# Optimization experiments

Measured on AMD Instinct MI355X. Metric: run time of the kernel, lower is better.

## Reference

```python
import jax, jax.numpy as jnp
import numpy as np

NUM_BRANCHES = 4
REP_DIM = 1024
FEAT_DIM = 128
N_DATA = 100000
NCE_K = 4096
NCE_T = 0.07
BATCH = 128
EPS = 1e-07


def setup_inputs() -> dict:
    key = jax.random.key(0)
    ks = jax.random.split(key, 8)
    d = {}
    for i in range(NUM_BRANCHES):
        d[f"emb{i}"] = jax.random.normal(ks[i], (BATCH, REP_DIM), dtype=jnp.float32)
    d["W"] = jax.random.normal(ks[4], (NUM_BRANCHES, FEAT_DIM, REP_DIM), dtype=jnp.float32) * 0.03
    d["b"] = jnp.zeros((NUM_BRANCHES, FEAT_DIM), dtype=jnp.float32)
    stdv = 1.0 / np.sqrt(FEAT_DIM / 3.0)
    d["memory"] = jax.random.uniform(ks[5], (NUM_BRANCHES, N_DATA, FEAT_DIM), dtype=jnp.float32, minval=-stdv, maxval=stdv)
    idx = jax.random.randint(ks[6], (BATCH,), 0, N_DATA)
    neg = jax.random.randint(ks[7], (BATCH, NCE_K), 0, N_DATA)
    d["idx"] = idx
    d["contrast_idx"] = jnp.concatenate([idx[:, None], neg], axis=1)  # col 0 = positive
    return d


def reference(emb0, emb1, emb2, emb3, W, b, memory, idx, contrast_idx):
    # per-branch Embed: flatten -> Linear -> L2 normalize
    embs = jnp.stack([emb0, emb1, emb2, emb3], axis=0)            # [R,B,rep]
    h = jnp.einsum('rbi,rdi->rbd', embs, W) + b[:, None, :]        # [R,B,D]
    e = h / jnp.sqrt(jnp.sum(h * h, axis=-1, keepdims=True))       # Normalize(power=2)

    # ContrastMemory: gather K+1 bank rows per sample per branch (detached)
    w = jax.lax.stop_gradient(memory[:, contrast_idx, :])          # [R,B,K+1,D]
    # scores[i,j,b,k] = <bank_j row, emb_i>  for every ordered pair
    scores = jnp.einsum('jbkd,ibd->ijbk', w, e)                    # [R,R,B,K+1]
    out = jnp.exp(scores / NCE_T)
    Z = jax.lax.stop_gradient(jnp.mean(out, axis=(2, 3)) * N_DATA)  # per-pair Z estimate
    out = out / Z[:, :, None, None]

    # ContrastLoss (Eq 11)
    m = float(NCE_K)
    Pn = 1.0 / float(N_DATA)
    pos = out[:, :, :, 0]                                          # [R,R,B]
    neg = out[:, :, :, 1:]                                         # [R,R,B,K]
    log_D1 = jnp.log(pos / (pos + m * Pn + EPS))
    log_D0 = jnp.log((m * Pn) / (neg + m * Pn + EPS))
    per_pair = -(jnp.sum(log_D1, axis=2) + jnp.sum(log_D0, axis=(2, 3))) / BATCH
    mask = 1.0 - jnp.eye(NUM_BRANCHES, dtype=per_pair.dtype)       # only i != j pairs
    return jnp.sum(per_pair * mask)
```

## Files before the change

kernel.cpp:

```cpp
#include <hip/hip_runtime.h>
#include <math.h>

#define NBR    4
#define REP    1024
#define FD     128
#define NDATA  100000
#define KP1    4097
#define BN     128
#define MPN    0.04096f
#define EPS_C  1e-7f
#define TINV   (1.0f / 0.07f)
#define NSLOT  64
#define TREFS  (BN * KP1)
#define NWAVE  8192

typedef unsigned int   uint4e   __attribute__((ext_vector_type(4)));
typedef unsigned short ushort4e __attribute__((ext_vector_type(4)));
typedef _Float16       half2e   __attribute__((ext_vector_type(2)));
typedef float          floatx4  __attribute__((ext_vector_type(4)));

static __device__ __forceinline__ unsigned short f2h(float f) {
    union { _Float16 h; unsigned short u; } c; c.h = (_Float16)f; return c.u;
}
static __device__ __forceinline__ float h_lo(unsigned int u) {
    union { unsigned int u; _Float16 h[2]; } c; c.u = u; return (float)c.h[0];
}
static __device__ __forceinline__ float h_hi(unsigned int u) {
    union { unsigned int u; _Float16 h[2]; } c; c.u = u; return (float)c.h[1];
}
static __device__ __forceinline__ half2e u2h2(unsigned int u) {
    union { unsigned int u; half2e h; } c; c.u = u; return c.h;
}
static __device__ __forceinline__ unsigned short f2bf(float f) {
    union { float f; unsigned int u; } c; c.f = f;
    unsigned int u = c.u;
    u += 0x7fffu + ((u >> 16) & 1u);
    return (unsigned short)(u >> 16);
}
static __device__ __forceinline__ float bf2f(unsigned short h) {
    union { unsigned int u; float f; } c; c.u = ((unsigned int)h) << 16;
    return c.f;
}

__global__ void k_feat(const float* __restrict__ e0, const float* __restrict__ e1,
                       const float* __restrict__ e2, const float* __restrict__ e3,
                       const float* __restrict__ W, const float* __restrict__ bias,
                       float* __restrict__ e_out, ushort* __restrict__ eh16) {
    const int r = blockIdx.x;
    const int b = blockIdx.y;
    const float* emb = (r == 0 ? e0 : r == 1 ? e1 : r == 2 ? e2 : e3) + (size_t)b * REP;

    __shared__ float s_emb[REP];
    for (int i = threadIdx.x; i < REP; i += blockDim.x) s_emb[i] = emb[i];
    __syncthreads();

    const int d = threadIdx.x;
    const float4* wrow = (const float4*)(W + ((size_t)r * FD + d) * REP);
    float acc = 0.f;
#pragma unroll 8
    for (int c = 0; c < REP / 4; ++c) {
        float4 v = wrow[c];
        acc += v.x * s_emb[4*c+0] + v.y * s_emb[4*c+1]
             + v.z * s_emb[4*c+2] + v.w * s_emb[4*c+3];
    }
    float h = acc + bias[r * FD + d];

    __shared__ float red[FD];
    red[d] = h * h;
    __syncthreads();
    for (int off = FD / 2; off > 0; off >>= 1) {
        if (d < off) red[d] += red[d + off];
        __syncthreads();
    }
    float nrm = sqrtf(red[0]);
    float val = h / nrm;
    e_out[((size_t)r * BN + b) * FD + d] = val;
    if (eh16) eh16[((size_t)r * BN + b) * FD + d] = f2h(val);
}

__global__ void k_hist(const int* __restrict__ cidx, int* __restrict__ counts) {
    const int k = blockIdx.x * 256 + threadIdx.x;
    if (k >= KP1) return;
    const int b = blockIdx.y;
    atomicAdd(&counts[cidx[(size_t)b * KP1 + k]], 1);
}

__global__ void k_assign(const int* __restrict__ counts, int* __restrict__ start,
                         int* __restrict__ cursor) {
    __shared__ int s[256];
    __shared__ int sbase;
    const int tid = threadIdx.x;
    const int n = blockIdx.x * 256 + tid;
    int c = (n < NDATA) ? counts[n] : 0;
    s[tid] = c;
    __syncthreads();
#pragma unroll
    for (int off = 1; off < 256; off <<= 1) {
        int v = (tid >= off) ? s[tid - off] : 0;
        __syncthreads();
        s[tid] += v;
        __syncthreads();
    }
    if (tid == 255) sbase = atomicAdd(cursor, s[255]);
    __syncthreads();
    if (n < NDATA) start[n] = sbase + s[tid] - c;
}

__global__ void k_scatter(const int* __restrict__ cidx, const int* __restrict__ start,
                          int* __restrict__ fill, unsigned long long* __restrict__ inv64) {
    const int k = blockIdx.x * 256 + threadIdx.x;
    if (k >= KP1) return;
    const int b = blockIdx.y;
    const int n = cidx[(size_t)b * KP1 + k];
    const int pos = atomicAdd(&fill[n], 1);
    inv64[(size_t)start[n] + pos] =
        ((unsigned long long)(unsigned int)n << 20) |
        ((unsigned long long)(unsigned int)b << 13) |
        (unsigned long long)(unsigned int)k;
}

__global__ __launch_bounds__(256)
void k_pass1i(const float* __restrict__ mem, const ushort* __restrict__ eh16,
              const unsigned long long* __restrict__ inv64,
              float* __restrict__ Zsl, ushort* __restrict__ expS) {
    const int lane = threadIdx.x & 63;
    const int w    = threadIdx.x >> 6;
    const int g    = (blockIdx.x << 2) + w;
    const int l4   = lane & 15;
    const int jj   = lane >> 4;
    const int d0   = l4 * 8;
    const bool b3  = (l4 & 8) != 0;
    const bool b2  = (l4 & 4) != 0;

    const int base = g * 64 + (g < 128 ? g : 128);
    const int end  = base + 64 + (g < 128 ? 1 : 0);

    const float* mrow_base = mem + (size_t)jj * NDATA * FD + d0;
    const ushort* eb_base  = eh16 + d0;

    float z = 0.f;
    int n_prev = -1;
    half2e mh[4];
    mh[0] = half2e{(_Float16)0.f, (_Float16)0.f};
    mh[1] = mh[0]; mh[2] = mh[0]; mh[3] = mh[0];

    unsigned long long vnext = inv64[base];
    for (int c = base; c < end; ++c) {
        const unsigned long long v = vnext;
        if (c + 1 < end) vnext = inv64[c + 1];
        const int n = (int)(v >> 20);
        const unsigned int bk = (unsigned int)v & 0xFFFFFu;
        const int b = (int)(bk >> 13);
        const int k = (int)(bk & 8191u);

        const ushort* eb = eb_base + (size_t)b * FD;
        uint4 ev0 = *(const uint4*)(eb);
        uint4 ev1 = *(const uint4*)(eb + (size_t)1 * BN * FD);
        uint4 ev2 = *(const uint4*)(eb + (size_t)2 * BN * FD);
        uint4 ev3 = *(const uint4*)(eb + (size_t)3 * BN * FD);

        if (n != n_prev) {
            const floatx4* mp = (const floatx4*)(mrow_base + (size_t)n * FD);
            floatx4 v0 = __builtin_nontemporal_load(mp);
            floatx4 v1 = __builtin_nontemporal_load(mp + 1);
            mh[0] = half2e{(_Float16)v0.x, (_Float16)v0.y};
            mh[1] = half2e{(_Float16)v0.z, (_Float16)v0.w};
            mh[2] = half2e{(_Float16)v1.x, (_Float16)v1.y};
            mh[3] = half2e{(_Float16)v1.z, (_Float16)v1.w};
            n_prev = n;
        }

        float a0 = 0.f, a1 = 0.f, a2 = 0.f, a3 = 0.f;
#pragma unroll
        for (int q = 0; q < 4; ++q) {
            half2e hw = mh[q];
            a0 = __builtin_amdgcn_fdot2(hw, u2h2((&ev0.x)[q]), a0, false);
            a1 = __builtin_amdgcn_fdot2(hw, u2h2((&ev1.x)[q]), a1, false);
            a2 = __builtin_amdgcn_fdot2(hw, u2h2((&ev2.x)[q]), a2, false);
            a3 = __builtin_amdgcn_fdot2(hw, u2h2((&ev3.x)[q]), a3, false);
        }
        float t0 = __shfl_xor(b3 ? a0 : a2, 8, 64);
        float t1 = __shfl_xor(b3 ? a1 : a3, 8, 64);
        float c0 = (b3 ? a2 : a0) + t0;
        float c1 = (b3 ? a3 : a1) + t1;
        float t2 = __shfl_xor(b2 ? c0 : c1, 4, 64);
        float d  = (b2 ? c1 : c0) + t2;
        d += __shfl_xor(d, 2, 64);
        d += __shfl_xor(d, 1, 64);
        float x = __expf(d * TINV);
        z += x;
        if ((lane & 3) == 0)
            expS[((size_t)b * KP1 + k) * 16 + (lane >> 2)] = f2h(x);
    }

    __shared__ float s_z[4][16];
    const int i = ((l4 >> 3) << 1) | ((l4 >> 2) & 1);
    if ((lane & 3) == 0) s_z[w][i * 4 + jj] = z;
    __syncthreads();
    if (threadIdx.x < 16) {
        float vv = s_z[0][threadIdx.x] + s_z[1][threadIdx.x]
                 + s_z[2][threadIdx.x] + s_z[3][threadIdx.x];
        const int slot = blockIdx.x & (NSLOT - 1);
        atomicAdd(&Zsl[slot * 16 + threadIdx.x], vv);
    }
}

__global__ void k_zred(const float* __restrict__ Zsl, float* __restrict__ Zsum) {
    if (threadIdx.x < 16) {
        float s = 0.f;
        for (int sl = 0; sl < NSLOT; ++sl) s += Zsl[sl * 16 + threadIdx.x];
        Zsum[threadIdx.x] = s;
    }
}

static __device__ __forceinline__ void acc_words(const uint4& p0, const uint4& p1,
                                                 const float* __restrict__ s_zinv,
                                                 float* __restrict__ acc, bool pos) {
    unsigned int wds[8] = {p0.x, p0.y, p0.z, p0.w, p1.x, p1.y, p1.z, p1.w};
#pragma unroll
    for (int w = 0; w < 8; ++w) {
        float v0 = h_lo(wds[w]) * s_zinv[2*w];
        float v1 = h_hi(wds[w]) * s_zinv[2*w+1];
        if (pos) {
            acc[2*w]   += -__logf(1.f + (MPN + EPS_C) / v0);
            acc[2*w+1] += -__logf(1.f + (MPN + EPS_C) / v1);
        } else {
            acc[2*w]   += -__logf(1.f + (v0 + EPS_C) * (1.f / MPN));
            acc[2*w+1] += -__logf(1.f + (v1 + EPS_C) * (1.f / MPN));
        }
    }
}

__global__ __launch_bounds__(256)
void k_pass2f(const uint4* __restrict__ expS, const float* __restrict__ Zsum,
              float* __restrict__ Asl) {
    const int b = blockIdx.y;

    __shared__ float s_zinv[16];
    if (threadIdx.x < 16) {
        int jj = threadIdx.x >> 2, ii = threadIdx.x & 3;
        float Z = Zsum[ii * 4 + jj] *
                  (float)((double)NDATA / ((double)BN * (double)KP1));
        s_zinv[threadIdx.x] = 1.0f / Z;
    }
    __syncthreads();

    const uint4* es = expS + (size_t)b * (KP1 * 2);
    const int base = threadIdx.x + blockIdx.x * 256;

    float acc[16];
#pragma unroll
    for (int t = 0; t < 16; ++t) acc[t] = 0.f;

#pragma unroll
    for (int it = 0; it < 2; ++it) {
        const int k = base + it * 2048;
        uint4 p0 = es[(size_t)k * 2];
        uint4 p1 = es[(size_t)k * 2 + 1];
        acc_words(p0, p1, s_zinv, acc, k == 0);
    }
    if (base == 0) {
        uint4 p0 = es[(size_t)4096 * 2];
        uint4 p1 = es[(size_t)4096 * 2 + 1];
        acc_words(p0, p1, s_zinv, acc, false);
    }

#pragma unroll
    for (int t = 0; t < 16; ++t) {
#pragma unroll
        for (int off = 32; off > 0; off >>= 1)
            acc[t] += __shfl_down(acc[t], off, 64);
    }
    __shared__ float s_a[4][16];
    const int w = threadIdx.x >> 6;
    if ((threadIdx.x & 63) == 0) {
#pragma unroll
        for (int t = 0; t < 16; ++t) s_a[w][t] = acc[t];
    }
    __syncthreads();
    if (threadIdx.x < 16) {
        float v = s_a[0][threadIdx.x] + s_a[1][threadIdx.x]
                + s_a[2][threadIdx.x] + s_a[3][threadIdx.x];
        const int slot = (blockIdx.y * gridDim.x + blockIdx.x) & (NSLOT - 1);
        atomicAdd(&Asl[slot * 16 + threadIdx.x], v);
    }
}

__global__ void k_final_slots(const float* __restrict__ Asl, float* __restrict__ out) {
    const int tid = threadIdx.x;
    const int comp = tid & 15;
    const int grp  = tid >> 4;
    float a = 0.f;
    for (int sl = grp; sl < NSLOT; sl += 16) a += Asl[sl * 16 + comp];
    const float m = ((comp >> 2) != (comp & 3)) ? 1.f : 0.f;
    __shared__ float s[256];
    s[tid] = a * m;
    __syncthreads();
    for (int off = 128; off > 0; off >>= 1) {
        if (tid < off) s[tid] += s[tid + off];
        __syncthreads();
    }
    if (tid == 0) out[0] = -s[0] / (float)BN;
}

static __device__ __forceinline__ void dot4(const float4* __restrict__ row,
                                            const float* __restrict__ se,
                                            float& a0, float& a1, float& a2, float& a3) {
    a0 = a1 = a2 = a3 = 0.f;
#pragma unroll 8
    for (int c = 0; c < FD / 4; ++c) {
        float4 v = row[c];
        const int o = 4 * c;
        a0 += v.x * se[0*FD+o+0] + v.y * se[0*FD+o+1] + v.z * se[0*FD+o+2] + v.w * se[0*FD+o+3];
        a1 += v.x * se[1*FD+o+0] + v.y * se[1*FD+o+1] + v.z * se[1*FD+o+2] + v.w * se[1*FD+o+3];
        a2 += v.x * se[2*FD+o+0] + v.y * se[2*FD+o+1] + v.z * se[2*FD+o+2] + v.w * se[2*FD+o+3];
        a3 += v.x * se[3*FD+o+0] + v.y * se[3*FD+o+1] + v.z * se[3*FD+o+2] + v.w * se[3*FD+o+3];
    }
}

static __device__ __forceinline__ void block_reduce4(float z0, float z1, float z2,
                                                     float z3, float* dst, int j) {
    __shared__ float sred[256];
    float zs[NBR] = {z0, z1, z2, z3};
    for (int i = 0; i < NBR; ++i) {
        sred[threadIdx.x] = zs[i];
        __syncthreads();
        for (int off = 128; off > 0; off >>= 1) {
            if ((int)threadIdx.x < off) sred[threadIdx.x] += sred[threadIdx.x + off];
            __syncthreads();
        }
        if (threadIdx.x == 0) atomicAdd(&dst[i * NBR + j], sred[0]);
        __syncthreads();
    }
}

static __device__ __forceinline__ float term_of(float ex, float zinv, int k) {
    const float c = MPN + EPS_C;
    float v = ex * zinv;
    if (k == 0) return -__logf(1.0f + c / v);
    return -__logf(1.0f + (v + EPS_C) * (1.0f / MPN));
}

template <bool STORE>
__global__ void k_pass1_f32(const float* __restrict__ e, const float* __restrict__ memory,
                            const int* __restrict__ cidx,
                            float* __restrict__ Zsum, ushort4* __restrict__ expS) {
    const int j = blockIdx.z;
    const int b = blockIdx.y;

    __shared__ float s_e[NBR * FD];
    for (int t = threadIdx.x; t < NBR * FD; t += blockDim.x) {
        int i = t >> 7, d = t & (FD - 1);
        s_e[t] = e[((size_t)i * BN + b) * FD + d];
    }
    __syncthreads();

    const int* ci = cidx + (size_t)b * KP1;
    const float4* mem4 = (const float4*)(memory + (size_t)j * NDATA * FD);
    float z0 = 0.f, z1 = 0.f, z2 = 0.f, z3 = 0.f;

    for (int k = threadIdx.x + blockIdx.x * blockDim.x; k < KP1;
         k += blockDim.x * gridDim.x) {
        const int n = ci[k];
        const float4* row = mem4 + (size_t)n * (FD / 4);
        float a0, a1, a2, a3;
        dot4(row, s_e, a0, a1, a2, a3);
        float x0 = __expf(a0 * TINV);
        float x1 = __expf(a1 * TINV);
        float x2 = __expf(a2 * TINV);
        float x3 = __expf(a3 * TINV);
        z0 += x0; z1 += x1; z2 += x2; z3 += x3;
        if (STORE) {
            ushort4 st;
            st.x = f2bf(x0); st.y = f2bf(x1); st.z = f2bf(x2); st.w = f2bf(x3);
            expS[((size_t)j * BN + b) * KP1 + k] = st;
        }
    }
    block_reduce4(z0, z1, z2, z3, Zsum, j);
}

__global__ void k_pass2_stored(const ushort4* __restrict__ expS,
                               const float* __restrict__ Zsum,
                               float* __restrict__ accum) {
    const int j = blockIdx.z;
    const int b = blockIdx.y;

    __shared__ float s_zinv[NBR];
    if (threadIdx.x < NBR) {
        float Z = Zsum[threadIdx.x * NBR + j] *
                  (float)((double)NDATA / ((double)BN * (double)KP1));
        s_zinv[threadIdx.x] = 1.0f / Z;
    }
    __syncthreads();

    const ushort4* es = expS + ((size_t)j * BN + b) * KP1;
    float a0 = 0.f, a1 = 0.f, a2 = 0.f, a3 = 0.f;

    for (int k = threadIdx.x + blockIdx.x * blockDim.x; k < KP1;
         k += blockDim.x * gridDim.x) {
        ushort4 v = es[k];
        a0 += term_of(bf2f(v.x), s_zinv[0], k);
        a1 += term_of(bf2f(v.y), s_zinv[1], k);
        a2 += term_of(bf2f(v.z), s_zinv[2], k);
        a3 += term_of(bf2f(v.w), s_zinv[3], k);
    }
    block_reduce4(a0, a1, a2, a3, accum, j);
}

__global__ void k_pass2_regather(const float* __restrict__ e, const float* __restrict__ memory,
                                 const int* __restrict__ cidx,
                                 const float* __restrict__ Zsum, float* __restrict__ accum) {
    const int j = blockIdx.z;
    const int b = blockIdx.y;

    __shared__ float s_e[NBR * FD];
    __shared__ float s_zinv[NBR];
    for (int t = threadIdx.x; t < NBR * FD; t += blockDim.x) {
        int i = t >> 7, d = t & (FD - 1);
        s_e[t] = e[((size_t)i * BN + b) * FD + d];
    }
    if (threadIdx.x < NBR) {
        float Z = Zsum[threadIdx.x * NBR + j] *
                  (float)((double)NDATA / ((double)BN * (double)KP1));
        s_zinv[threadIdx.x] = 1.0f / Z;
    }
    __syncthreads();

    const int* ci = cidx + (size_t)b * KP1;
    const float4* mem4 = (const float4*)(memory + (size_t)j * NDATA * FD);
    float a0s = 0.f, a1s = 0.f, a2s = 0.f, a3s = 0.f;

    for (int k = threadIdx.x + blockIdx.x * blockDim.x; k < KP1;
         k += blockDim.x * gridDim.x) {
        const int n = ci[k];
        const float4* row = mem4 + (size_t)n * (FD / 4);
        float a0, a1, a2, a3;
        dot4(row, s_e, a0, a1, a2, a3);
        a0s += term_of(__expf(a0 * TINV), s_zinv[0], k);
        a1s += term_of(__expf(a1 * TINV), s_zinv[1], k);
        a2s += term_of(__expf(a2 * TINV), s_zinv[2], k);
        a3s += term_of(__expf(a3 * TINV), s_zinv[3], k);
    }
    block_reduce4(a0s, a1s, a2s, a3s, accum, j);
}

__global__ void k_init(float* __restrict__ p, int n) {
    int i = blockIdx.x * blockDim.x + threadIdx.x;
    if (i < n) p[i] = 0.f;
}

__global__ void k_final_legacy(const float* __restrict__ accum, float* __restrict__ out) {
    if (threadIdx.x == 0) {
        float s = 0.f;
        for (int i = 0; i < NBR; ++i)
            for (int j = 0; j < NBR; ++j)
                if (i != j) s += -accum[i * NBR + j] / (float)BN;
        out[0] = s;
    }
}

extern "C" void kernel_launch(void* const* d_in, const int* in_sizes, int n_in,
                              void* d_out, int out_size, void* d_ws, size_t ws_size,
                              hipStream_t stream) {
    const float* e0   = (const float*)d_in[0];
    const float* e1   = (const float*)d_in[1];
    const float* e2   = (const float*)d_in[2];
    const float* e3   = (const float*)d_in[3];
    const float* W    = (const float*)d_in[4];
    const float* bias = (const float*)d_in[5];
    const float* mem  = (const float*)d_in[6];
    const int*   cidx = (const int*)d_in[8];
    float* out = (float*)d_out;

    float* ws    = (float*)d_ws;
    float* e     = ws;
    float* Zsum  = ws + 65536;
    float* accum = ws + 65552;
    float* Zsl   = ws + 65568;
    float* Asl   = ws + 66592;
    const size_t base_b   = (size_t)67616 * 4;
    const size_t eh16_b   = (size_t)NBR * BN * FD * 2;
    const size_t cnt_b    = (size_t)NDATA * 4;
    const size_t cur_b    = 16;
    const size_t inv_b    = (size_t)TREFS * 8;
    const size_t expS_b   = (size_t)BN * KP1 * 16 * 2;

    const size_t off_eh16   = base_b;
    const size_t off_counts = off_eh16 + eh16_b;
    const size_t off_fill   = off_counts + cnt_b;
    const size_t off_cursor = off_fill + cnt_b;
    const size_t off_start  = off_cursor + cur_b;
    const size_t off_inv    = off_start + cnt_b;
    const size_t off_expS   = off_inv + inv_b;

    const size_t need_full = off_expS + expS_b;
    const size_t need_mid  = base_b + expS_b;

    if (ws_size >= need_full) {
        ushort* eh16 = (ushort*)((char*)d_ws + off_eh16);
        int* counts  = (int*)((char*)d_ws + off_counts);
        int* fill    = (int*)((char*)d_ws + off_fill);
        int* cursor  = (int*)((char*)d_ws + off_cursor);
        int* start   = (int*)((char*)d_ws + off_start);
        unsigned long long* inv64 = (unsigned long long*)((char*)d_ws + off_inv);
        ushort* expS = (ushort*)((char*)d_ws + off_expS);

        k_init<<<9, 256, 0, stream>>>(Zsum, 2080);
        k_init<<<782, 256, 0, stream>>>((float*)counts, 200004);
        k_feat<<<dim3(NBR, BN), 128, 0, stream>>>(e0, e1, e2, e3, W, bias, e, eh16);
        k_hist<<<dim3(17, BN), 256, 0, stream>>>(cidx, counts);
        k_assign<<<391, 256, 0, stream>>>(counts, start, cursor);
        k_scatter<<<dim3(17, BN), 256, 0, stream>>>(cidx, start, fill, inv64);
        k_pass1i<<<2048, 256, 0, stream>>>(mem, eh16, inv64, Zsl, expS);
        k_zred<<<1, 64, 0, stream>>>(Zsl, Zsum);
        k_pass2f<<<dim3(8, BN), 256, 0, stream>>>((const uint4*)expS, Zsum, Asl);
        k_final_slots<<<1, 256, 0, stream>>>(Asl, out);
    } else if (ws_size >= need_mid) {
        k_init<<<9, 256, 0, stream>>>(Zsum, 2080);
        k_feat<<<dim3(NBR, BN), 128, 0, stream>>>(e0, e1, e2, e3, W, bias, e, nullptr);
        ushort4* expS = (ushort4*)((char*)d_ws + base_b);
        k_pass1_f32<true><<<dim3(4, BN, NBR), 256, 0, stream>>>(e, mem, cidx, Zsum, expS);
        k_pass2_stored<<<dim3(4, BN, NBR), 256, 0, stream>>>(expS, Zsum, accum);
        k_final_legacy<<<1, 64, 0, stream>>>(accum, out);
    } else {
        k_init<<<9, 256, 0, stream>>>(Zsum, 2080);
        k_feat<<<dim3(NBR, BN), 128, 0, stream>>>(e0, e1, e2, e3, W, bias, e, nullptr);
        k_pass1_f32<false><<<dim3(4, BN, NBR), 256, 0, stream>>>(e, mem, cidx, Zsum, nullptr);
        k_pass2_regather<<<dim3(4, BN, NBR), 256, 0, stream>>>(e, mem, cidx, Zsum, accum);
        k_final_legacy<<<1, 64, 0, stream>>>(accum, out);
    }
}
```

Measured before the change: 484.2 us.

## Fuse setup kernels, store exp scores in sorted order, and software-pipeline pass-1 gathers

The launch sequence goes from ten kernels to six. Init is merged, the feature projection runs in the same launch as the histogram, and the Z reduction and final sum are folded into a single grid-stride pass-2 that adds into the output atomically. Pass-1 now writes exp scores in sorted order, so its stores are contiguous, and it stores embeddings interleaved by branch so that each lane does four contiguous 16-byte loads. It also prefetches two entries ahead, keeping memory rows and embedding vectors in flight. Positives are handled by recording their sorted positions and applying a correction term, which adds some bookkeeping and an order-dependent float atomic sum.

```diff
diff --git a/kernel.cpp b/kernel.cpp
--- a/kernel.cpp
+++ b/kernel.cpp
@@ -12,12 +12,9 @@
 #define TINV   (1.0f / 0.07f)
 #define NSLOT  64
 #define TREFS  (BN * KP1)
-#define NWAVE  8192
-
-typedef unsigned int   uint4e   __attribute__((ext_vector_type(4)));
-typedef unsigned short ushort4e __attribute__((ext_vector_type(4)));
-typedef _Float16       half2e   __attribute__((ext_vector_type(2)));
-typedef float          floatx4  __attribute__((ext_vector_type(4)));
+
+typedef _Float16 half2e  __attribute__((ext_vector_type(2)));
+typedef float    floatx4 __attribute__((ext_vector_type(4)));
 
 static __device__ __forceinline__ unsigned short f2h(float f) {
     union { _Float16 h; unsigned short u; } c; c.h = (_Float16)f; return c.u;
@@ -42,10 +39,337 @@
     return c.f;
 }
 
+__global__ void k_init2(int* __restrict__ cnts, float* __restrict__ Zsl,
+                        float* __restrict__ out) {
+    const int i = blockIdx.x * 256 + threadIdx.x;
+    if (i < 200004) cnts[i] = 0;
+    if (i < NSLOT * 16) Zsl[i] = 0.f;
+    if (i == 0) out[0] = 0.f;
+}
+
+__global__ __launch_bounds__(256)
+void k_fh(const float* __restrict__ e0, const float* __restrict__ e1,
+          const float* __restrict__ e2, const float* __restrict__ e3,
+          const float* __restrict__ W, const float* __restrict__ bias,
+          const int* __restrict__ cidx,
+          ushort* __restrict__ eh2, int* __restrict__ counts) {
+    const int tid = threadIdx.x;
+    if ((int)blockIdx.x < NBR * BN) {
+        __shared__ float s_emb[REP];
+        __shared__ float s_part[256];
+        __shared__ float s_sq[FD];
+        const int u = blockIdx.x;
+        const int r = u >> 7;
+        const int b = u & 127;
+        const float* emb = (r == 0 ? e0 : r == 1 ? e1 : r == 2 ? e2 : e3)
+                           + (size_t)b * REP;
+        for (int t = tid; t < REP; t += 256) s_emb[t] = emb[t];
+        __syncthreads();
+        const int d  = tid & 127;
+        const int kh = tid >> 7;
+        const float4* wrow = (const float4*)(W + ((size_t)r * FD + d) * REP)
+                             + kh * 128;
+        const float* se = s_emb + (kh << 9);
+        float a = 0.f;
+#pragma unroll 4
+        for (int c = 0; c < 128; ++c) {
+            float4 v = wrow[c];
+            a += v.x * se[4*c+0] + v.y * se[4*c+1]
+               + v.z * se[4*c+2] + v.w * se[4*c+3];
+        }
+        s_part[tid] = a;
+        __syncthreads();
+        float h = 0.f;
+        if (kh == 0) {
+            h = s_part[d] + s_part[128 + d] + bias[r * FD + d];
+            s_sq[d] = h * h;
+        }
+        __syncthreads();
+        for (int off = 64; off > 0; off >>= 1) {
+            if (tid < off) s_sq[tid] += s_sq[tid + off];
+            __syncthreads();
+        }
+        float nrm = sqrtf(s_sq[0]);
+        if (kh == 0) {
+            eh2[((size_t)(b * 16 + (d >> 3)) * 4 + r) * 8 + (d & 7)]
+                = f2h(h / nrm);
+        }
+    } else {
+        const int NT = 256 * 256;
+        for (int t = ((int)blockIdx.x - NBR * BN) * 256 + tid; t < TREFS; t += NT)
+            atomicAdd(&counts[cidx[t]], 1);
+    }
+}
+
+__global__ void k_assign(const int* __restrict__ counts, int* __restrict__ start,
+                         int* __restrict__ cursor) {
+    __shared__ int s[256];
+    __shared__ int sbase;
+    const int tid = threadIdx.x;
+    const int n = blockIdx.x * 256 + tid;
+    int c = (n < NDATA) ? counts[n] : 0;
+    s[tid] = c;
+    __syncthreads();
+#pragma unroll
+    for (int off = 1; off < 256; off <<= 1) {
+        int v = (tid >= off) ? s[tid - off] : 0;
+        __syncthreads();
+        s[tid] += v;
+        __syncthreads();
+    }
+    if (tid == 255) sbase = atomicAdd(cursor, s[255]);
+    __syncthreads();
+    if (n < NDATA) start[n] = sbase + s[tid] - c;
+}
+
+__global__ void k_scatter(const int* __restrict__ cidx, const int* __restrict__ start,
+                          int* __restrict__ fill, unsigned long long* __restrict__ inv64,
+                          int* __restrict__ posc) {
+    const int k = blockIdx.x * 256 + threadIdx.x;
+    if (k >= KP1) return;
+    const int b = blockIdx.y;
+    const int n = cidx[(size_t)b * KP1 + k];
+    const int pos = atomicAdd(&fill[n], 1);
+    const int c = start[n] + pos;
+    inv64[c] =
+        ((unsigned long long)(unsigned int)n << 20) |
+        ((unsigned long long)(unsigned int)b << 13) |
+        (unsigned long long)(unsigned int)k;
+    if (k == 0) posc[b] = c;
+}
+
+__global__ __launch_bounds__(256)
+void k_pass1i(const float* __restrict__ mem, const ushort* __restrict__ eh2,
+              const unsigned long long* __restrict__ inv64,
+              float* __restrict__ Zsl, ushort* __restrict__ expS) {
+    const int tid  = threadIdx.x;
+    const int lane = tid & 63;
+    const int wv   = tid >> 6;
+    const int g    = ((int)blockIdx.x << 2) + wv;
+    const int l4   = lane & 15;
+    const int jj   = lane >> 4;
+    const bool f3  = (l4 & 8) != 0;
+    const bool fl2 = (l4 & 4) != 0;
+
+    const int base = g * 64 + (g < 128 ? g : 128);
+    const int end  = base + 64 + (g < 128 ? 1 : 0);
+
+    const float* mrow = mem + (size_t)jj * (NDATA * FD) + l4 * 8;
+    const uint4* e4   = (const uint4*)eh2;
+
+    float z = 0.f;
+
+    half2e mh0 = half2e{(_Float16)0.f, (_Float16)0.f};
+    half2e mh1 = mh0, mh2 = mh0, mh3 = mh0;
+    floatx4 pr0, pr1;
+    int cur_n = -1;
+
+    unsigned long long v0 = inv64[base];
+    unsigned long long v1 = inv64[base + 1];
+    unsigned long long v2 = (base + 2 < end) ? inv64[base + 2] : v1;
+    unsigned long long v3 = (base + 3 < end) ? inv64[base + 3] : v2;
+
+    uint4 qA0, qA1, qA2, qA3, qB0, qB1, qB2, qB3;
+    {
+        const uint4* p = e4 + ((size_t)(((unsigned)v0 & 0xFFFFFu) >> 13) * 16 + l4) * 4;
+        qA0 = p[0]; qA1 = p[1]; qA2 = p[2]; qA3 = p[3];
+    }
+    {
+        const uint4* p = e4 + ((size_t)(((unsigned)v1 & 0xFFFFFu) >> 13) * 16 + l4) * 4;
+        qB0 = p[0]; qB1 = p[1]; qB2 = p[2]; qB3 = p[3];
+    }
+
+    int pend_n = (int)(v0 >> 20);
+    {
+        const floatx4* mp = (const floatx4*)(mrow + (size_t)pend_n * FD);
+        pr0 = __builtin_nontemporal_load(mp);
+        pr1 = __builtin_nontemporal_load(mp + 1);
+    }
+
+    auto cvt = [&]() {
+        mh0 = half2e{(_Float16)pr0.x, (_Float16)pr0.y};
+        mh1 = half2e{(_Float16)pr0.z, (_Float16)pr0.w};
+        mh2 = half2e{(_Float16)pr1.x, (_Float16)pr1.y};
+        mh3 = half2e{(_Float16)pr1.z, (_Float16)pr1.w};
+    };
+    auto ldrow = [&](int n) {
+        const floatx4* mp = (const floatx4*)(mrow + (size_t)n * FD);
+        pr0 = __builtin_nontemporal_load(mp);
+        pr1 = __builtin_nontemporal_load(mp + 1);
+        pend_n = n;
+    };
+    auto proc = [&](int cc, const uint4& q0, const uint4& q1,
+                    const uint4& q2, const uint4& q3) {
+        float a0 = 0.f, a1 = 0.f, a2 = 0.f, a3 = 0.f;
+        a0 = __builtin_amdgcn_fdot2(mh0, u2h2(q0.x), a0, false);
+        a0 = __builtin_amdgcn_fdot2(mh1, u2h2(q0.y), a0, false);
+        a0 = __builtin_amdgcn_fdot2(mh2, u2h2(q0.z), a0, false);
+        a0 = __builtin_amdgcn_fdot2(mh3, u2h2(q0.w), a0, false);
+        a1 = __builtin_amdgcn_fdot2(mh0, u2h2(q1.x), a1, false);
+        a1 = __builtin_amdgcn_fdot2(mh1, u2h2(q1.y), a1, false);
+        a1 = __builtin_amdgcn_fdot2(mh2, u2h2(q1.z), a1, false);
+        a1 = __builtin_amdgcn_fdot2(mh3, u2h2(q1.w), a1, false);
+        a2 = __builtin_amdgcn_fdot2(mh0, u2h2(q2.x), a2, false);
+        a2 = __builtin_amdgcn_fdot2(mh1, u2h2(q2.y), a2, false);
+        a2 = __builtin_amdgcn_fdot2(mh2, u2h2(q2.z), a2, false);
+        a2 = __builtin_amdgcn_fdot2(mh3, u2h2(q2.w), a2, false);
+        a3 = __builtin_amdgcn_fdot2(mh0, u2h2(q3.x), a3, false);
+        a3 = __builtin_amdgcn_fdot2(mh1, u2h2(q3.y), a3, false);
+        a3 = __builtin_amdgcn_fdot2(mh2, u2h2(q3.z), a3, false);
+        a3 = __builtin_amdgcn_fdot2(mh3, u2h2(q3.w), a3, false);
+        float t0 = __shfl_xor(f3 ? a0 : a2, 8, 64);
+        float t1 = __shfl_xor(f3 ? a1 : a3, 8, 64);
+        float c0 = (f3 ? a2 : a0) + t0;
+        float c1 = (f3 ? a3 : a1) + t1;
+        float t2 = __shfl_xor(fl2 ? c0 : c1, 4, 64);
+        float dd = (fl2 ? c1 : c0) + t2;
+        dd += __shfl_xor(dd, 2, 64);
+        dd += __shfl_xor(dd, 1, 64);
+        float x = __expf(dd * TINV);
+        z += x;
+        if ((lane & 3) == 0)
+            expS[(size_t)cc * 16 + (lane >> 2)] = f2h(x);
+    };
+
+    int c = base;
+    for (; c + 1 < end; c += 2) {
+        const int n0 = (int)(v0 >> 20);
+        if (n0 != cur_n) {
+            if (n0 != pend_n) ldrow(n0);
+            cvt();
+            cur_n = n0;
+        }
+        const int n1 = (int)(v1 >> 20);
+        if (n1 != cur_n && n1 != pend_n) ldrow(n1);
+        proc(c, qA0, qA1, qA2, qA3);
+        {
+            const uint4* p = e4 + ((size_t)(((unsigned)v2 & 0xFFFFFu) >> 13) * 16 + l4) * 4;
+            qA0 = p[0]; qA1 = p[1]; qA2 = p[2]; qA3 = p[3];
+        }
+        if (n1 != cur_n) { cvt(); cur_n = n1; }
+        const int n2 = (int)(v2 >> 20);
+        if (n2 != cur_n && n2 != pend_n) ldrow(n2);
+        proc(c + 1, qB0, qB1, qB2, qB3);
+        {
+            const uint4* p = e4 + ((size_t)(((unsigned)v3 & 0xFFFFFu) >> 13) * 16 + l4) * 4;
+            qB0 = p[0]; qB1 = p[1]; qB2 = p[2]; qB3 = p[3];
+        }
+        v0 = v2; v1 = v3;
+        v2 = (c + 4 < end) ? inv64[c + 4] : v3;
+        v3 = (c + 5 < end) ? inv64[c + 5] : v2;
+    }
+    if (c < end) {
+        const int n0 = (int)(v0 >> 20);
+        if (n0 != cur_n) {
+            if (n0 != pend_n) ldrow(n0);
+            cvt();
+            cur_n = n0;
+        }
+        proc(c, qA0, qA1, qA2, qA3);
+    }
+
+    __shared__ float s_z[4][16];
+    const int i = ((l4 >> 3) << 1) | ((l4 >> 2) & 1);
+    if ((lane & 3) == 0) s_z[wv][i * 4 + jj] = z;
+    __syncthreads();
+    if (tid < 16) {
+        float vv = s_z[0][tid] + s_z[1][tid] + s_z[2][tid] + s_z[3][tid];
+        const int slot = blockIdx.x & (NSLOT - 1);
+        atomicAdd(&Zsl[slot * 16 + tid], vv);
+    }
+}
+
+__global__ __launch_bounds__(256)
+void k_pass2s(const uint4* __restrict__ esu, const float* __restrict__ Zsl,
+              const int* __restrict__ posc, float* __restrict__ out) {
+    const int tid = threadIdx.x;
+    __shared__ float s_zinv[16];
+    if (tid < 16) {
+        const int comp = ((tid & 3) << 2) | (tid >> 2);
+        float s = 0.f;
+        for (int sl = 0; sl < NSLOT; ++sl) s += Zsl[sl * 16 + comp];
+        float Z = s * (float)((double)NDATA / ((double)BN * (double)KP1));
+        s_zinv[tid] = 1.0f / Z;
+    }
+    __syncthreads();
+
+    float acc[16];
+#pragma unroll
+    for (int t = 0; t < 16; ++t) acc[t] = 0.f;
+
+    const int NT = gridDim.x * 256;
+    for (int t = blockIdx.x * 256 + tid; t < TREFS; t += NT) {
+        uint4 p0 = esu[(size_t)t * 2];
+        uint4 p1 = esu[(size_t)t * 2 + 1];
+        unsigned int wds[8] = {p0.x, p0.y, p0.z, p0.w, p1.x, p1.y, p1.z, p1.w};
+#pragma unroll
+        for (int w = 0; w < 8; ++w) {
+            float v0 = h_lo(wds[w]) * s_zinv[2*w];
+            float v1 = h_hi(wds[w]) * s_zinv[2*w+1];
+            acc[2*w]   += -__logf(1.f + (v0 + EPS_C) * (1.f / MPN));
+            acc[2*w+1] += -__logf(1.f + (v1 + EPS_C) * (1.f / MPN));
+        }
+    }
+
+#pragma unroll
+    for (int t = 0; t < 16; ++t) {
+#pragma unroll
+        for (int off = 32; off > 0; off >>= 1)
+            acc[t] += __shfl_down(acc[t], off, 64);
+    }
+    __shared__ float s_a[4][16];
+    const int wv = tid >> 6;
+    if ((tid & 63) == 0) {
+#pragma unroll
+        for (int t = 0; t < 16; ++t) s_a[wv][t] = acc[t];
+    }
+    __syncthreads();
+    if (tid < 16) {
+        float v = s_a[0][tid] + s_a[1][tid] + s_a[2][tid] + s_a[3][tid];
+        v = ((tid >> 2) != (tid & 3)) ? v : 0.f;
+        v += __shfl_down(v, 8, 64);
+        v += __shfl_down(v, 4, 64);
+        v += __shfl_down(v, 2, 64);
+        v += __shfl_down(v, 1, 64);
+        if (tid == 0) atomicAdd(out, -v / (float)BN);
+    }
+
+    if (blockIdx.x == 0) {
+        float corr = 0.f;
+        if (tid < BN) {
+            const int cc = posc[tid];
+            uint4 p0 = esu[(size_t)cc * 2];
+            uint4 p1 = esu[(size_t)cc * 2 + 1];
+            unsigned int wds[8] = {p0.x, p0.y, p0.z, p0.w, p1.x, p1.y, p1.z, p1.w};
+#pragma unroll
+            for (int w = 0; w < 8; ++w) {
+#pragma unroll
+                for (int hl = 0; hl < 2; ++hl) {
+                    const int h = 2 * w + hl;
+                    if ((h >> 2) != (h & 3)) {
+                        float val = hl ? h_hi(wds[w]) : h_lo(wds[w]);
+                        float v = val * s_zinv[h];
+                        float posT = -__logf(1.f + (MPN + EPS_C) / v);
+                        float negT = -__logf(1.f + (v + EPS_C) * (1.f / MPN));
+                        corr += posT - negT;
+                    }
+                }
+            }
+        }
+        for (int off = 32; off > 0; off >>= 1)
+            corr += __shfl_down(corr, off, 64);
+        __shared__ float s_c[4];
+        if ((tid & 63) == 0) s_c[wv] = corr;
+        __syncthreads();
+        if (tid == 0)
+            atomicAdd(out, -(s_c[0] + s_c[1] + s_c[2] + s_c[3]) / (float)BN);
+    }
+}
+
 __global__ void k_feat(const float* __restrict__ e0, const float* __restrict__ e1,
                        const float* __restrict__ e2, const float* __restrict__ e3,
                        const float* __restrict__ W, const float* __restrict__ bias,
-                       float* __restrict__ e_out, ushort* __restrict__ eh16) {
+                       float* __restrict__ e_out) {
     const int r = blockIdx.x;
     const int b = blockIdx.y;
     const float* emb = (r == 0 ? e0 : r == 1 ? e1 : r == 2 ? e2 : e3) + (size_t)b * REP;
@@ -73,234 +397,7 @@
         __syncthreads();
     }
     float nrm = sqrtf(red[0]);
-    float val = h / nrm;
-    e_out[((size_t)r * BN + b) * FD + d] = val;
-    if (eh16) eh16[((size_t)r * BN + b) * FD + d] = f2h(val);
-}
-
-__global__ void k_hist(const int* __restrict__ cidx, int* __restrict__ counts) {
-    const int k = blockIdx.x * 256 + threadIdx.x;
-    if (k >= KP1) return;
-    const int b = blockIdx.y;
-    atomicAdd(&counts[cidx[(size_t)b * KP1 + k]], 1);
-}
-
-__global__ void k_assign(const int* __restrict__ counts, int* __restrict__ start,
-                         int* __restrict__ cursor) {
-    __shared__ int s[256];
-    __shared__ int sbase;
-    const int tid = threadIdx.x;
-    const int n = blockIdx.x * 256 + tid;
-    int c = (n < NDATA) ? counts[n] : 0;
-    s[tid] = c;
-    __syncthreads();
-#pragma unroll
-    for (int off = 1; off < 256; off <<= 1) {
-        int v = (tid >= off) ? s[tid - off] : 0;
-        __syncthreads();
-        s[tid] += v;
-        __syncthreads();
-    }
-    if (tid == 255) sbase = atomicAdd(cursor, s[255]);
-    __syncthreads();
-    if (n < NDATA) start[n] = sbase + s[tid] - c;
-}
-
-__global__ void k_scatter(const int* __restrict__ cidx, const int* __restrict__ start,
-                          int* __restrict__ fill, unsigned long long* __restrict__ inv64) {
-    const int k = blockIdx.x * 256 + threadIdx.x;
-    if (k >= KP1) return;
-    const int b = blockIdx.y;
-    const int n = cidx[(size_t)b * KP1 + k];
-    const int pos = atomicAdd(&fill[n], 1);
-    inv64[(size_t)start[n] + pos] =
-        ((unsigned long long)(unsigned int)n << 20) |
-        ((unsigned long long)(unsigned int)b << 13) |
-        (unsigned long long)(unsigned int)k;
-}
-
-__global__ __launch_bounds__(256)
-void k_pass1i(const float* __restrict__ mem, const ushort* __restrict__ eh16,
-              const unsigned long long* __restrict__ inv64,
-              float* __restrict__ Zsl, ushort* __restrict__ expS) {
-    const int lane = threadIdx.x & 63;
-    const int w    = threadIdx.x >> 6;
-    const int g    = (blockIdx.x << 2) + w;
-    const int l4   = lane & 15;
-    const int jj   = lane >> 4;
-    const int d0   = l4 * 8;
-    const bool b3  = (l4 & 8) != 0;
-    const bool b2  = (l4 & 4) != 0;
-
-    const int base = g * 64 + (g < 128 ? g : 128);
-    const int end  = base + 64 + (g < 128 ? 1 : 0);
-
-    const float* mrow_base = mem + (size_t)jj * NDATA * FD + d0;
-    const ushort* eb_base  = eh16 + d0;
-
-    float z = 0.f;
-    int n_prev = -1;
-    half2e mh[4];
-    mh[0] = half2e{(_Float16)0.f, (_Float16)0.f};
-    mh[1] = mh[0]; mh[2] = mh[0]; mh[3] = mh[0];
-
-    unsigned long long vnext = inv64[base];
-    for (int c = base; c < end; ++c) {
-        const unsigned long long v = vnext;
-        if (c + 1 < end) vnext = inv64[c + 1];
-        const int n = (int)(v >> 20);
-        const unsigned int bk = (unsigned int)v & 0xFFFFFu;
-        const int b = (int)(bk >> 13);
-        const int k = (int)(bk & 8191u);
-
-        const ushort* eb = eb_base + (size_t)b * FD;
-        uint4 ev0 = *(const uint4*)(eb);
-        uint4 ev1 = *(const uint4*)(eb + (size_t)1 * BN * FD);
-        uint4 ev2 = *(const uint4*)(eb + (size_t)2 * BN * FD);
-        uint4 ev3 = *(const uint4*)(eb + (size_t)3 * BN * FD);
-
-        if (n != n_prev) {
-            const floatx4* mp = (const floatx4*)(mrow_base + (size_t)n * FD);
-            floatx4 v0 = __builtin_nontemporal_load(mp);
-            floatx4 v1 = __builtin_nontemporal_load(mp + 1);
-            mh[0] = half2e{(_Float16)v0.x, (_Float16)v0.y};
-            mh[1] = half2e{(_Float16)v0.z, (_Float16)v0.w};
-            mh[2] = half2e{(_Float16)v1.x, (_Float16)v1.y};
-            mh[3] = half2e{(_Float16)v1.z, (_Float16)v1.w};
-            n_prev = n;
-        }
-
-        float a0 = 0.f, a1 = 0.f, a2 = 0.f, a3 = 0.f;
-#pragma unroll
-        for (int q = 0; q < 4; ++q) {
-            half2e hw = mh[q];
-            a0 = __builtin_amdgcn_fdot2(hw, u2h2((&ev0.x)[q]), a0, false);
-            a1 = __builtin_amdgcn_fdot2(hw, u2h2((&ev1.x)[q]), a1, false);
-            a2 = __builtin_amdgcn_fdot2(hw, u2h2((&ev2.x)[q]), a2, false);
-            a3 = __builtin_amdgcn_fdot2(hw, u2h2((&ev3.x)[q]), a3, false);
-        }
-        float t0 = __shfl_xor(b3 ? a0 : a2, 8, 64);
-        float t1 = __shfl_xor(b3 ? a1 : a3, 8, 64);
-        float c0 = (b3 ? a2 : a0) + t0;
-        float c1 = (b3 ? a3 : a1) + t1;
-        float t2 = __shfl_xor(b2 ? c0 : c1, 4, 64);
-        float d  = (b2 ? c1 : c0) + t2;
-        d += __shfl_xor(d, 2, 64);
-        d += __shfl_xor(d, 1, 64);
-        float x = __expf(d * TINV);
-        z += x;
-        if ((lane & 3) == 0)
-            expS[((size_t)b * KP1 + k) * 16 + (lane >> 2)] = f2h(x);
-    }
-
-    __shared__ float s_z[4][16];
-    const int i = ((l4 >> 3) << 1) | ((l4 >> 2) & 1);
-    if ((lane & 3) == 0) s_z[w][i * 4 + jj] = z;
-    __syncthreads();
-    if (threadIdx.x < 16) {
-        float vv = s_z[0][threadIdx.x] + s_z[1][threadIdx.x]
-                 + s_z[2][threadIdx.x] + s_z[3][threadIdx.x];
-        const int slot = blockIdx.x & (NSLOT - 1);
-        atomicAdd(&Zsl[slot * 16 + threadIdx.x], vv);
-    }
-}
-
-__global__ void k_zred(const float* __restrict__ Zsl, float* __restrict__ Zsum) {
-    if (threadIdx.x < 16) {
-        float s = 0.f;
-        for (int sl = 0; sl < NSLOT; ++sl) s += Zsl[sl * 16 + threadIdx.x];
-        Zsum[threadIdx.x] = s;
-    }
-}
-
-static __device__ __forceinline__ void acc_words(const uint4& p0, const uint4& p1,
-                                                 const float* __restrict__ s_zinv,
-                                                 float* __restrict__ acc, bool pos) {
-    unsigned int wds[8] = {p0.x, p0.y, p0.z, p0.w, p1.x, p1.y, p1.z, p1.w};
-#pragma unroll
-    for (int w = 0; w < 8; ++w) {
-        float v0 = h_lo(wds[w]) * s_zinv[2*w];
-        float v1 = h_hi(wds[w]) * s_zinv[2*w+1];
-        if (pos) {
-            acc[2*w]   += -__logf(1.f + (MPN + EPS_C) / v0);
-            acc[2*w+1] += -__logf(1.f + (MPN + EPS_C) / v1);
-        } else {
-            acc[2*w]   += -__logf(1.f + (v0 + EPS_C) * (1.f / MPN));
-            acc[2*w+1] += -__logf(1.f + (v1 + EPS_C) * (1.f / MPN));
-        }
-    }
-}
-
-__global__ __launch_bounds__(256)
-void k_pass2f(const uint4* __restrict__ expS, const float* __restrict__ Zsum,
-              float* __restrict__ Asl) {
-    const int b = blockIdx.y;
-
-    __shared__ float s_zinv[16];
-    if (threadIdx.x < 16) {
-        int jj = threadIdx.x >> 2, ii = threadIdx.x & 3;
-        float Z = Zsum[ii * 4 + jj] *
-                  (float)((double)NDATA / ((double)BN * (double)KP1));
-        s_zinv[threadIdx.x] = 1.0f / Z;
-    }
-    __syncthreads();
-
-    const uint4* es = expS + (size_t)b * (KP1 * 2);
-    const int base = threadIdx.x + blockIdx.x * 256;
-
-    float acc[16];
-#pragma unroll
-    for (int t = 0; t < 16; ++t) acc[t] = 0.f;
-
-#pragma unroll
-    for (int it = 0; it < 2; ++it) {
-        const int k = base + it * 2048;
-        uint4 p0 = es[(size_t)k * 2];
-        uint4 p1 = es[(size_t)k * 2 + 1];
-        acc_words(p0, p1, s_zinv, acc, k == 0);
-    }
-    if (base == 0) {
-        uint4 p0 = es[(size_t)4096 * 2];
-        uint4 p1 = es[(size_t)4096 * 2 + 1];
-        acc_words(p0, p1, s_zinv, acc, false);
-    }
-
-#pragma unroll
-    for (int t = 0; t < 16; ++t) {
-#pragma unroll
-        for (int off = 32; off > 0; off >>= 1)
-            acc[t] += __shfl_down(acc[t], off, 64);
-    }
-    __shared__ float s_a[4][16];
-    const int w = threadIdx.x >> 6;
-    if ((threadIdx.x & 63) == 0) {
-#pragma unroll
-        for (int t = 0; t < 16; ++t) s_a[w][t] = acc[t];
-    }
-    __syncthreads();
-    if (threadIdx.x < 16) {
-        float v = s_a[0][threadIdx.x] + s_a[1][threadIdx.x]
-                + s_a[2][threadIdx.x] + s_a[3][threadIdx.x];
-        const int slot = (blockIdx.y * gridDim.x + blockIdx.x) & (NSLOT - 1);
-        atomicAdd(&Asl[slot * 16 + threadIdx.x], v);
-    }
-}
-
-__global__ void k_final_slots(const float* __restrict__ Asl, float* __restrict__ out) {
-    const int tid = threadIdx.x;
-    const int comp = tid & 15;
-    const int grp  = tid >> 4;
-    float a = 0.f;
-    for (int sl = grp; sl < NSLOT; sl += 16) a += Asl[sl * 16 + comp];
-    const float m = ((comp >> 2) != (comp & 3)) ? 1.f : 0.f;
-    __shared__ float s[256];
-    s[tid] = a * m;
-    __syncthreads();
-    for (int off = 128; off > 0; off >>= 1) {
-        if (tid < off) s[tid] += s[tid + off];
-        __syncthreads();
-    }
-    if (tid == 0) out[0] = -s[0] / (float)BN;
+    e_out[((size_t)r * BN + b) * FD + d] = h / nrm;
 }
 
 static __device__ __forceinline__ void dot4(const float4* __restrict__ row,
@@ -477,56 +574,52 @@
     float* Zsum  = ws + 65536;
     float* accum = ws + 65552;
     float* Zsl   = ws + 65568;
-    float* Asl   = ws + 66592;
-    const size_t base_b   = (size_t)67616 * 4;
-    const size_t eh16_b   = (size_t)NBR * BN * FD * 2;
-    const size_t cnt_b    = (size_t)NDATA * 4;
-    const size_t cur_b    = 16;
-    const size_t inv_b    = (size_t)TREFS * 8;
-    const size_t expS_b   = (size_t)BN * KP1 * 16 * 2;
-
-    const size_t off_eh16   = base_b;
-    const size_t off_counts = off_eh16 + eh16_b;
+    const size_t base_b  = (size_t)67616 * 4;
+    const size_t cnt_b   = (size_t)NDATA * 4;
+    const size_t inv_b   = (size_t)TREFS * 8;
+    const size_t expS_b  = (size_t)TREFS * 16 * 2;
+    const size_t eh2_b   = (size_t)BN * 16 * 4 * 8 * 2;
+
+    const size_t off_counts = base_b;
     const size_t off_fill   = off_counts + cnt_b;
     const size_t off_cursor = off_fill + cnt_b;
-    const size_t off_start  = off_cursor + cur_b;
+    const size_t off_start  = off_cursor + 16;
     const size_t off_inv    = off_start + cnt_b;
     const size_t off_expS   = off_inv + inv_b;
-
-    const size_t need_full = off_expS + expS_b;
+    const size_t off_eh2    = off_expS + expS_b;
+    const size_t off_posc   = off_eh2 + eh2_b;
+
+    const size_t need_main = off_posc + 512;
     const size_t need_mid  = base_b + expS_b;
 
-    if (ws_size >= need_full) {
-        ushort* eh16 = (ushort*)((char*)d_ws + off_eh16);
+    if (ws_size >= need_main) {
         int* counts  = (int*)((char*)d_ws + off_counts);
         int* fill    = (int*)((char*)d_ws + off_fill);
         int* cursor  = (int*)((char*)d_ws + off_cursor);
         int* start   = (int*)((char*)d_ws + off_start);
         unsigned long long* inv64 = (unsigned long long*)((char*)d_ws + off_inv);
         ushort* expS = (ushort*)((char*)d_ws + off_expS);
-
-        k_init<<<9, 256, 0, stream>>>(Zsum, 2080);
-        k_init<<<782, 256, 0, stream>>>((float*)counts, 200004);
-        k_feat<<<dim3(NBR, BN), 128, 0, stream>>>(e0, e1, e2, e3, W, bias, e, eh16);
-        k_hist<<<dim3(17, BN), 256, 0, stream>>>(cidx, counts);
+        ushort* eh2  = (ushort*)((char*)d_ws + off_eh2);
+        int* posc    = (int*)((char*)d_ws + off_posc);
+
+        k_init2<<<782, 256, 0, stream>>>(counts, Zsl, out);
+        k_fh<<<NBR * BN + 256, 256, 0, stream>>>(e0, e1, e2, e3, W, bias, cidx,
+                                                 eh2, counts);
         k_assign<<<391, 256, 0, stream>>>(counts, start, cursor);
-        k_scatter<<<dim3(17, BN), 256, 0, stream>>>(cidx, start, fill, inv64);
-        k_pass1i<<<2048, 256, 0, stream>>>(mem, eh16, inv64, Zsl, expS);
-        k_zred<<<1, 64, 0, stream>>>(Zsl, Zsum);
-        k_pass2f<<<dim3(8, BN), 256, 0, stream>>>((const uint4*)expS, Zsum, Asl);
-        k_final_slots<<<1, 256, 0, stream>>>(Asl, out);
-    } else if (ws_size >= need_mid) {
-        k_init<<<9, 256, 0, stream>>>(Zsum, 2080);
-        k_feat<<<dim3(NBR, BN), 128, 0, stream>>>(e0, e1, e2, e3, W, bias, e, nullptr);
-        ushort4* expS = (ushort4*)((char*)d_ws + base_b);
-        k_pass1_f32<true><<<dim3(4, BN, NBR), 256, 0, stream>>>(e, mem, cidx, Zsum, expS);
-        k_pass2_stored<<<dim3(4, BN, NBR), 256, 0, stream>>>(expS, Zsum, accum);
-        k_final_legacy<<<1, 64, 0, stream>>>(accum, out);
+        k_scatter<<<dim3(17, BN), 256, 0, stream>>>(cidx, start, fill, inv64, posc);
+        k_pass1i<<<2048, 256, 0, stream>>>(mem, eh2, inv64, Zsl, expS);
+        k_pass2s<<<1024, 256, 0, stream>>>((const uint4*)expS, Zsl, posc, out);
     } else {
         k_init<<<9, 256, 0, stream>>>(Zsum, 2080);
-        k_feat<<<dim3(NBR, BN), 128, 0, stream>>>(e0, e1, e2, e3, W, bias, e, nullptr);
-        k_pass1_f32<false><<<dim3(4, BN, NBR), 256, 0, stream>>>(e, mem, cidx, Zsum, nullptr);
-        k_pass2_regather<<<dim3(4, BN, NBR), 256, 0, stream>>>(e, mem, cidx, Zsum, accum);
+        k_feat<<<dim3(NBR, BN), 128, 0, stream>>>(e0, e1, e2, e3, W, bias, e);
+        if (ws_size >= need_mid) {
+            ushort4* expS = (ushort4*)((char*)d_ws + base_b);
+            k_pass1_f32<true><<<dim3(4, BN, NBR), 256, 0, stream>>>(e, mem, cidx, Zsum, expS);
+            k_pass2_stored<<<dim3(4, BN, NBR), 256, 0, stream>>>(expS, Zsum, accum);
+        } else {
+            k_pass1_f32<false><<<dim3(4, BN, NBR), 256, 0, stream>>>(e, mem, cidx, Zsum, nullptr);
+            k_pass2_regather<<<dim3(4, BN, NBR), 256, 0, stream>>>(e, mem, cidx, Zsum, accum);
+        }
         k_final_legacy<<<1, 64, 0, stream>>>(accum, out);
     }
 }
```

After: 525.4 us. 1.09x slower.
